# Kernel optimization log

Measured on AMD Instinct MI355X. Metric: run time of the kernel, lower is better.

## Reference

```python
import jax, jax.numpy as jnp
import numpy as np

Q_HEADS, KV_HEADS, DIMS, IN_DIMS = 16, 4, 1024, 1024
HEAD_D = DIMS // Q_HEADS            # 64
GROUPS = Q_HEADS // KV_HEADS        # 4
ROPE_BASE = 10000.0


def nd_rope(x, coords):
    """N-D rotary embedding.
    x: [..., s, d]; coords: broadcastable [..., s, a] (float).
    Head dim d is split into a contiguous chunks of d//a; within each chunk
    consecutive pairs (2i, 2i+1) are rotated by angle coord_axis * base^(-2i/(d//a)).
    """
    a = coords.shape[-1]
    d = x.shape[-1]
    dpa = d // a                                  # dims per coordinate axis (even)
    inv_freq = ROPE_BASE ** (-jnp.arange(dpa // 2, dtype=jnp.float32) * (2.0 / dpa))
    angles = coords[..., :, None] * inv_freq      # [..., s, a, dpa//2]
    angles = angles.reshape(angles.shape[:-2] + (d // 2,))
    cos, sin = jnp.cos(angles), jnp.sin(angles)
    xp = x.reshape(x.shape[:-1] + (d // 2, 2))
    x1, x2 = xp[..., 0], xp[..., 1]
    return jnp.stack([x1 * cos - x2 * sin, x1 * sin + x2 * cos], axis=-1).reshape(x.shape)


def setup_inputs() -> dict:
    key = jax.random.key(0)
    k1, k2, k3, k4, k5, k6, k7, k8 = jax.random.split(key, 8)
    B, SQ, SKV, A = 4, 2048, 2048, 2
    q = jax.random.normal(k1, (B, SQ, IN_DIMS), dtype=jnp.float32)
    kv = jax.random.normal(k2, (B, SKV, IN_DIMS), dtype=jnp.float32)
    q_coords = jax.random.randint(k3, (B, SQ, A), 0, 2048, dtype=jnp.int32)
    kv_coords = jax.random.randint(k4, (B, SKV, A), 0, 2048, dtype=jnp.int32)
    s_in = 1.0 / np.sqrt(IN_DIMS)
    Wq = jax.random.normal(k5, (IN_DIMS, Q_HEADS, HEAD_D), dtype=jnp.float32) * s_in
    Wk = jax.random.normal(k6, (IN_DIMS, KV_HEADS, HEAD_D), dtype=jnp.float32) * s_in
    Wv = jax.random.normal(k7, (IN_DIMS, KV_HEADS, HEAD_D), dtype=jnp.float32) * s_in
    Wo = jax.random.normal(k8, (KV_HEADS * HEAD_D, IN_DIMS), dtype=jnp.float32) * (1.0 / np.sqrt(KV_HEADS * HEAD_D))
    return {"q": q, "q_coords": q_coords, "kv": kv, "kv_coords": kv_coords,
            "Wq": Wq, "Wk": Wk, "Wv": Wv, "Wo": Wo}


def reference(q, q_coords, kv, kv_coords, Wq, Wk, Wv, Wo):
    B, SQ = q.shape[0], q.shape[1]
    qp = jnp.einsum('bsi,ihd->bshd', q, Wq)   # [b, sq, q_heads, hd]
    kp = jnp.einsum('bsi,ihd->bshd', kv, Wk)  # [b, skv, kv_heads, hd]
    vp = jnp.einsum('bsi,ihd->bshd', kv, Wv)
    # '... s (h g) d -> ... g h s d' with h=KV_HEADS outer, g=GROUPS inner
    qp = qp.reshape(B, SQ, KV_HEADS, GROUPS, HEAD_D).transpose(0, 3, 2, 1, 4)  # [b,g,h,sq,hd]
    kp = kp.transpose(0, 2, 1, 3)  # [b,h,skv,hd]
    vp = vp.transpose(0, 2, 1, 3)
    qc = q_coords.astype(jnp.float32)[:, None, None]  # [b,1,1,sq,a] -> broadcast over g,h
    kc = kv_coords.astype(jnp.float32)[:, None]       # [b,1,skv,a] -> broadcast over h
    qr = nd_rope(qp, qc)
    kr = nd_rope(kp, kc)
    # NOTE: einops pattern omits g in output -> group axis is SUMMED (faithful to source)
    scores = jnp.einsum('bghsd,bhad->bhsa', qr, kr) / (HEAD_D ** 0.5)
    attn = jax.nn.softmax(scores, axis=-1)
    out = jnp.einsum('bhsa,bhad->bhsd', attn, vp)
    out = out.transpose(0, 2, 1, 3).reshape(B, SQ, KV_HEADS * HEAD_D)
    return out @ Wo
```

## Files before the change

### kernel.cpp

```cpp
#include <hip/hip_runtime.h>

#define BATCH 4
#define SEQQ  2048
#define SEQKV 2048
#define NH    4
#define HD    64
#define IND   1024
#define QSCL 0.18033688011112042f

typedef __attribute__((ext_vector_type(8))) short short8;
typedef __attribute__((ext_vector_type(4))) short s4v;
typedef __attribute__((ext_vector_type(4))) float floatx4;

#if defined(__HIP_DEVICE_COMPILE__) && __has_builtin(__builtin_amdgcn_exp2f)
  #define EXP2(x) __builtin_amdgcn_exp2f(x)
#else
  #define EXP2(x) exp2f(x)
#endif

#if defined(__HIP_DEVICE_COMPILE__)
  #if __has_builtin(__builtin_amdgcn_mfma_f32_16x16x16bf16_1k)
    #define MFMA16(a, b, c) __builtin_amdgcn_mfma_f32_16x16x16bf16_1k(a, b, c, 0, 0, 0)
  #elif __has_builtin(__builtin_amdgcn_mfma_f32_16x16x16_bf16)
    #define MFMA16(a, b, c) __builtin_amdgcn_mfma_f32_16x16x16_bf16(a, b, c, 0, 0, 0)
  #else
    #error "no 16x16x16 bf16 MFMA builtin on gfx950 device pass"
  #endif
#else
  #define MFMA16(a, b, c) (c)
#endif
#define MFMA32(a, b, c) __builtin_amdgcn_mfma_f32_16x16x32_bf16(a, b, c, 0, 0, 0)

__device__ __forceinline__ short f2b(float f) {
    unsigned u; __builtin_memcpy(&u, &f, 4);
    u = (u + 0x7fffu + ((u >> 16) & 1u)) >> 16;
    return (short)u;
}
__device__ __forceinline__ short8 cvt8(const float* p) {
    float4 a = *(const float4*)p;
    float4 b = *(const float4*)(p + 4);
    short8 r;
    r[0] = f2b(a.x); r[1] = f2b(a.y); r[2] = f2b(a.z); r[3] = f2b(a.w);
    r[4] = f2b(b.x); r[5] = f2b(b.y); r[6] = f2b(b.z); r[7] = f2b(b.w);
    return r;
}

__global__ __launch_bounds__(256) void prep_all(
    const float* __restrict__ Wq, const float* __restrict__ Wk,
    const float* __restrict__ Wv, const float* __restrict__ Wo,
    const float* __restrict__ q, const float* __restrict__ kv,
    short* __restrict__ Wq_t, short* __restrict__ Wkv_t, short* __restrict__ Wo_t,
    short* __restrict__ qb, short* __restrict__ kvb) {
    __shared__ short Ts[64][65];
    int blk = blockIdx.x;
    if (blk < 256) {
        int c4 = threadIdx.x & 63, r4 = threadIdx.x >> 6;
        if (blk < 64) {
            int h = blk & 3, ib = blk >> 2;
#pragma unroll 4
            for (int jj = 0; jj < 16; ++jj) {
                int il = r4 * 16 + jj;
                float s = 0.f;
#pragma unroll
                for (int g = 0; g < 4; ++g)
                    s += Wq[(ib * 64 + il) * 1024 + (h * 4 + g) * 64 + c4];
                Ts[il][c4] = f2b(s);
            }
            __syncthreads();
#pragma unroll 4
            for (int jj = 0; jj < 16; ++jj) {
                int dl = r4 * 16 + jj;
                Wq_t[(h * 64 + dl) * 1024 + ib * 64 + c4] = Ts[c4][dl];
            }
        } else if (blk < 192) {
            int t = blk - 64, ss = t >> 6; t &= 63;
            int ib = t >> 2, nb = t & 3;
            const float* W = ss ? Wv : Wk;
#pragma unroll 4
            for (int jj = 0; jj < 16; ++jj) {
                int il = r4 * 16 + jj;
                Ts[il][c4] = f2b(W[(ib * 64 + il) * 256 + nb * 64 + c4]);
            }
            __syncthreads();
#pragma unroll 4
            for (int jj = 0; jj < 16; ++jj) {
                int dl = r4 * 16 + jj;
                Wkv_t[(ss * 256 + nb * 64 + dl) * 1024 + ib * 64 + c4] = Ts[c4][dl];
            }
        } else {
            int t = blk - 192, kb = t >> 4, nb = t & 15;
#pragma unroll 4
            for (int jj = 0; jj < 16; ++jj) {
                int il = r4 * 16 + jj;
                Ts[il][c4] = f2b(Wo[(kb * 64 + il) * 1024 + nb * 64 + c4]);
            }
            __syncthreads();
#pragma unroll 4
            for (int jj = 0; jj < 16; ++jj) {
                int dl = r4 * 16 + jj;
                Wo_t[(nb * 64 + dl) * 256 + kb * 64 + c4] = Ts[c4][dl];
            }
        }
    } else if (blk < 2304) {
        long e = ((long)(blk - 256) * 256 + threadIdx.x) * 16;
        *(short8*)(qb + e)     = cvt8(q + e);
        *(short8*)(qb + e + 8) = cvt8(q + e + 8);
    } else {
        long e = ((long)(blk - 2304) * 256 + threadIdx.x) * 16;
        *(short8*)(kvb + e)     = cvt8(kv + e);
        *(short8*)(kvb + e + 8) = cvt8(kv + e + 8);
    }
}

template <int MODE>
__device__ __forceinline__ void gemm64(
    const short* __restrict__ A, const short* __restrict__ Wt,
    int m0, int n0, short* As, short* Bs,
    const int* __restrict__ coords, short* __restrict__ ropeDst,
    short* __restrict__ vDst) {
    const int t = threadIdx.x;
    const int w = t >> 6, lane = t & 63, ln = lane & 15, quad = lane >> 4;
    const int srow = lane >> 2, skc = (lane & 3) * 8;
    floatx4 acc[2][4];
#pragma unroll
    for (int mt = 0; mt < 2; ++mt)
#pragma unroll
        for (int nt = 0; nt < 4; ++nt) acc[mt][nt] = floatx4{0.f, 0.f, 0.f, 0.f};

    auto stage = [&](int ks, int sel) {
#pragma unroll
        for (int i = 0; i < 2; ++i)
            __builtin_amdgcn_global_load_lds(
                (const void*)(A + (long)(m0 + w * 32 + i * 16 + srow) * 1024 + ks + skc),
                (void*)(As + sel * 4096 + (w * 2 + i) * 512), 16, 0, 0);
        __builtin_amdgcn_global_load_lds(
            (const void*)(Wt + (long)(n0 + w * 16 + srow) * 1024 + ks + skc),
            (void*)(Bs + sel * 2048 + w * 512), 16, 0, 0);
    };

    stage(0, 0);
    __syncthreads();
    int cur = 0;
    for (int tt = 0; tt < 32; ++tt) {
        if (tt < 31) stage((tt + 1) * 32, cur ^ 1);
        const short* Ac = As + cur * 4096;
        const short* Bc = Bs + cur * 2048;
        short8 af[2], bf[4];
#pragma unroll
        for (int mt = 0; mt < 2; ++mt)
            af[mt] = *(const short8*)(Ac + (w * 32 + mt * 16 + ln) * 32 + quad * 8);
#pragma unroll
        for (int nt = 0; nt < 4; ++nt)
            bf[nt] = *(const short8*)(Bc + (nt * 16 + ln) * 32 + quad * 8);
#pragma unroll
        for (int mt = 0; mt < 2; ++mt)
#pragma unroll
            for (int nt = 0; nt < 4; ++nt)
                acc[mt][nt] = MFMA32(af[mt], bf[nt], acc[mt][nt]);
        __syncthreads();
        cur ^= 1;
    }

    if (MODE == 1 || n0 < 256) {
        const int h = (n0 >> 6) & 3;
        const float scl = (MODE == 1) ? QSCL : 1.0f;
        const float L = -0.5756462732485114f;
        const float fA = __expf((float)(ln >> 1) * L);
        const float fB = __expf((float)(8 + (ln >> 1)) * L);
        const float sgn = (ln & 1) ? 1.0f : -1.0f;
#pragma unroll
        for (int mt = 0; mt < 2; ++mt) {
            int row0 = m0 + w * 32 + mt * 16 + quad * 4;
#pragma unroll
            for (int r = 0; r < 4; ++r) {
                int row = row0 + r;
                float c0 = (float)coords[row * 2];
                float c1 = (float)coords[row * 2 + 1];
                float snv[4], csv[4];
                __sincosf(c0 * fA, &snv[0], &csv[0]);
                __sincosf(c0 * fB, &snv[1], &csv[1]);
                __sincosf(c1 * fA, &snv[2], &csv[2]);
                __sincosf(c1 * fB, &snv[3], &csv[3]);
                long rbase = ((long)((row >> 11) * 4 + h) * 2048 + (row & 2047)) * 64;
#pragma unroll
                for (int nt = 0; nt < 4; ++nt) {
                    float v = acc[mt][nt][r];
                    float p = __shfl_xor(v, 1, 64);
                    float o = v * (csv[nt] * scl) + p * (snv[nt] * (scl * sgn));
                    ropeDst[rbase + nt * 16 + ln] = f2b(o);
                }
            }
        }
    } else {
        const int h = ((n0 - 256) >> 6) & 3;
#pragma unroll
        for (int mt = 0; mt < 2; ++mt) {
            int row0 = m0 + w * 32 + mt * 16 + quad * 4;
            int b = row0 >> 11, s0 = row0 & 2047;
#pragma unroll
            for (int nt = 0; nt < 4; ++nt) {
                s4v ov;
#pragma unroll
                for (int r = 0; r < 4; ++r) ov[r] = f2b(acc[mt][nt][r]);
                *(s4v*)(vDst + (long)((b * 4 + h) * 64 + nt * 16 + ln) * 2048 + s0) = ov;
            }
        }
    }
}

__global__ __launch_bounds__(256) void proj_gemm(
    const short* __restrict__ qb, const short* __restrict__ kvb,
    const short* __restrict__ Wq_t, const short* __restrict__ Wkv_t,
    const int* __restrict__ qc, const int* __restrict__ kvc,
    short* __restrict__ Qr, short* __restrict__ Kr, short* __restrict__ Vt) {
    __shared__ __align__(16) short As[2 * 4096];
    __shared__ __align__(16) short Bs[2 * 2048];
    int id = (blockIdx.x & 7) * 96 + (blockIdx.x >> 3);
    if (id < 256)
        gemm64<1>(qb, Wq_t, (id >> 2) * 128, (id & 3) * 64, As, Bs, qc, Qr, nullptr);
    else {
        int t2 = id - 256;
        gemm64<2>(kvb, Wkv_t, (t2 >> 3) * 128, (t2 & 7) * 64, As, Bs, kvc, Kr, Vt);
    }
}

__global__ __launch_bounds__(256) void final_gemm(
    const short* __restrict__ Ob, const short* __restrict__ Wo_t, float* __restrict__ out) {
    __shared__ __align__(16) short As[2][128 * 32];
    __shared__ __align__(16) short Bs[2][128 * 32];
    const int m0 = blockIdx.x * 128, n0 = blockIdx.y * 128;
    const int tid = threadIdx.x;
    const int w = tid >> 6, lane = tid & 63, ln = lane & 15, quad = lane >> 4;
    const int wm = w >> 1, wn = w & 1;
    const int srow = lane >> 2, skc = (lane & 3) * 8;
    floatx4 acc[4][4];
#pragma unroll
    for (int mt = 0; mt < 4; ++mt)
#pragma unroll
        for (int nt = 0; nt < 4; ++nt) acc[mt][nt] = floatx4{0.f, 0.f, 0.f, 0.f};

    auto stage = [&](int ks, int sel) {
#pragma unroll
        for (int i = 0; i < 2; ++i) {
            __builtin_amdgcn_global_load_lds(
                (const void*)(Ob + (long)(m0 + w * 32 + i * 16 + srow) * 256 + ks + skc),
                (void*)(&As[sel][(w * 2 + i) * 512]), 16, 0, 0);
            __builtin_amdgcn_global_load_lds(
                (const void*)(Wo_t + (long)(n0 + w * 32 + i * 16 + srow) * 256 + ks + skc),
                (void*)(&Bs[sel][(w * 2 + i) * 512]), 16, 0, 0);
        }
    };
    stage(0, 0);
    __syncthreads();
    int cur = 0;
    for (int tt = 0; tt < 8; ++tt) {
        if (tt < 7) stage((tt + 1) * 32, cur ^ 1);
        const short* Ac = &As[cur][0];
        const short* Bc = &Bs[cur][0];
        short8 af[4], bf[4];
#pragma unroll
        for (int mt = 0; mt < 4; ++mt)
            af[mt] = *(const short8*)(Ac + (wm * 64 + mt * 16 + ln) * 32 + quad * 8);
#pragma unroll
        for (int nt = 0; nt < 4; ++nt)
            bf[nt] = *(const short8*)(Bc + (wn * 64 + nt * 16 + ln) * 32 + quad * 8);
#pragma unroll
        for (int mt = 0; mt < 4; ++mt)
#pragma unroll
            for (int nt = 0; nt < 4; ++nt)
                acc[mt][nt] = MFMA32(af[mt], bf[nt], acc[mt][nt]);
        __syncthreads();
        cur ^= 1;
    }
#pragma unroll
    for (int mt = 0; mt < 4; ++mt) {
        int row0 = m0 + wm * 64 + mt * 16 + quad * 4;
#pragma unroll
        for (int nt = 0; nt < 4; ++nt) {
            int col = n0 + wn * 64 + nt * 16 + ln;
#pragma unroll
            for (int r = 0; r < 4; ++r)
                out[(long)(row0 + r) * 1024 + col] = acc[mt][nt][r];
        }
    }
}

__global__ __launch_bounds__(512, 4) void attn_kernel(
    const short* __restrict__ Qr, const short* __restrict__ Kr,
    const short* __restrict__ Vt, short* __restrict__ Ob) {
    __shared__ __align__(16) short Kls[2][2][64 * 64];
    __shared__ __align__(16) short Vls[2][2][64 * 64];
    const int blk = blockIdx.x;
    const int x = blk & 7, y = blk >> 3;
    const int bh = x * 2 + (y >> 5), qg = y & 31;
    const int w = threadIdx.x >> 6, lane = threadIdx.x & 63;
    const int qw = w & 3, half = w >> 2;
    const int ln = lane & 15, quad = lane >> 4;
    const int q0 = qg * 64 + qw * 16;
    const short* Qb = Qr + (long)bh * SEQKV * HD;
    const short* Kb = Kr + (long)bh * SEQKV * HD + (long)half * 1024 * HD;
    const short* Vb = Vt + (long)bh * HD * SEQKV + half * 1024;

    const int srow = lane >> 3;
    const int schk = (lane & 7) ^ (srow & 7);
    const long kstage0 = (long)(qw * 16 + srow) * HD + schk * 8;
    const long vstage0 = (long)(qw * 16 + srow) * SEQKV + schk * 8;

    short8 qf[2];
#pragma unroll
    for (int ck = 0; ck < 2; ++ck)
        qf[ck] = *(const short8*)(Qb + (long)(q0 + ln) * HD + ck * 32 + quad * 8);

    s4v ones;
#pragma unroll
    for (int j = 0; j < 4; ++j) ones[j] = (short)0x3F80;

    floatx4 o[4], ol;
    ol = floatx4{0.f, 0.f, 0.f, 0.f};
#pragma unroll
    for (int nt = 0; nt < 4; ++nt) o[nt] = floatx4{0.f, 0.f, 0.f, 0.f};

    const int ln7 = ln & 7;
    int koff[2];
#pragma unroll
    for (int ck = 0; ck < 2; ++ck) koff[ck] = ln * 64 + ((ck * 4 + quad) ^ ln7) * 8;
    int voff[4];
#pragma unroll
    for (int t = 0; t < 4; ++t) voff[t] = ln * 64 + ((t * 2 + (quad >> 1)) ^ ln7) * 8 + (quad & 1) * 4;

#define STAGE(kt, sel)                                                                \
    do {                                                                              \
        _Pragma("unroll")                                                             \
        for (int i = 0; i < 2; ++i) {                                                 \
            __builtin_amdgcn_global_load_lds(                                         \
                (const void*)(Kb + (long)(kt) * HD + kstage0 + (long)i * 8 * HD),     \
                (void*)(&Kls[half][sel][(qw * 16 + i * 8) * 64]), 16, 0, 0);          \
            __builtin_amdgcn_global_load_lds(                                         \
                (const void*)(Vb + (kt) + vstage0 + (long)i * 8 * SEQKV),             \
                (void*)(&Vls[half][sel][(qw * 16 + i * 8) * 64]), 16, 0, 0);          \
        }                                                                             \
    } while (0)

    STAGE(0, 0);
    __syncthreads();
    int cur = 0;
    for (int tt = 0; tt < 16; ++tt) {
        if (tt < 15) STAGE((tt + 1) * 64, cur ^ 1);
        const short* Kc = &Kls[half][cur][0];
        const short* Vc = &Vls[half][cur][0];
#pragma unroll
        for (int t = 0; t < 4; ++t) {
            short8 a0 = *(const short8*)(Kc + t * 1024 + koff[0]);
            short8 a1 = *(const short8*)(Kc + t * 1024 + koff[1]);
            floatx4 st = {0.f, 0.f, 0.f, 0.f};
            __builtin_amdgcn_s_setprio(1);
            st = MFMA32(a0, qf[0], st);
            st = MFMA32(a1, qf[1], st);
            __builtin_amdgcn_s_setprio(0);
            float e0 = EXP2(st[0]), e1 = EXP2(st[1]), e2 = EXP2(st[2]), e3 = EXP2(st[3]);
            unsigned p0, p1;
            asm("v_cvt_pk_bf16_f32 %0, %1, %2" : "=v"(p0) : "v"(e0), "v"(e1));
            asm("v_cvt_pk_bf16_f32 %0, %1, %2" : "=v"(p1) : "v"(e2), "v"(e3));
            s4v pt;
            { unsigned tmp[2] = {p0, p1}; __builtin_memcpy(&pt, tmp, 8); }
            __builtin_amdgcn_s_setprio(1);
#pragma unroll
            for (int nt = 0; nt < 4; ++nt) {
                s4v vf = *(const s4v*)(Vc + nt * 1024 + voff[t]);
                o[nt] = MFMA16(vf, pt, o[nt]);
            }
            ol = MFMA16(ones, pt, ol);
            __builtin_amdgcn_s_setprio(0);
        }
        __syncthreads();
        cur ^= 1;
    }
#undef STAGE
    float* cb = (float*)&Kls[0][0][0];
    const int slot = (qw * 64 + lane) * 20;
    if (half == 1) {
#pragma unroll
        for (int nt = 0; nt < 4; ++nt)
            *(floatx4*)(cb + slot + nt * 4) = o[nt];
        cb[slot + 16] = ol[0];
    }
    __syncthreads();
    if (half == 0) {
        const int b = bh >> 2, h = bh & 3;
        const float li = 1.0f / (ol[0] + cb[slot + 16]);
        const long base = ((long)(b * 2048 + q0 + ln)) * 256 + h * 64;
#pragma unroll
        for (int nt = 0; nt < 4; ++nt) {
            floatx4 o2 = *(const floatx4*)(cb + slot + nt * 4);
            s4v ov;
#pragma unroll
            for (int r = 0; r < 4; ++r) ov[r] = f2b((o[nt][r] + o2[r]) * li);
            *(s4v*)(Ob + base + nt * 16 + quad * 4) = ov;
        }
    }
}

extern "C" void kernel_launch(void* const* d_in, const int* in_sizes, int n_in,
                              void* d_out, int out_size, void* d_ws, size_t ws_size,
                              hipStream_t stream) {
    const float* q   = (const float*)d_in[0];
    const int*   qc  = (const int*)d_in[1];
    const float* kv  = (const float*)d_in[2];
    const int*   kvc = (const int*)d_in[3];
    const float* Wq  = (const float*)d_in[4];
    const float* Wk  = (const float*)d_in[5];
    const float* Wv  = (const float*)d_in[6];
    const float* Wo  = (const float*)d_in[7];
    float* out = (float*)d_out;

    char* ws = (char*)d_ws;
    const size_t MB = 1024 * 1024;
    short* Wq_t  = (short*)(ws);
    short* Wkv_t = (short*)(ws + MB / 2);
    short* Wo_t  = (short*)(ws + 3 * MB / 2);
    short* qb    = (short*)(ws + 2 * MB);
    short* kvb   = (short*)(ws + 18 * MB);
    short* Qr    = (short*)(ws + 34 * MB);
    short* Kr    = (short*)(ws + 38 * MB);
    short* Vt    = (short*)(ws + 42 * MB);
    short* Ob    = (short*)(ws + 46 * MB);

    hipLaunchKernelGGL(prep_all, dim3(4352), dim3(256), 0, stream,
                       Wq, Wk, Wv, Wo, q, kv, Wq_t, Wkv_t, Wo_t, qb, kvb);
    hipLaunchKernelGGL(proj_gemm, dim3(768), dim3(256), 0, stream,
                       qb, kvb, Wq_t, Wkv_t, qc, kvc, Qr, Kr, Vt);
    hipLaunchKernelGGL(attn_kernel, dim3(512), dim3(512), 0, stream,
                       Qr, Kr, Vt, Ob);
    hipLaunchKernelGGL(final_gemm, dim3(64, 8), dim3(256), 0, stream, Ob, Wo_t, out);
}
```

Baseline: 188.7 us.

## Widen GEMM K-tile to 64 with XOR-swizzled LDS layout in projection and output GEMMs

Both the projection GEMM and the final output GEMM now stage 64-wide K slices instead of 32, which halves the number of main-loop iterations and barriers. The LDS layout gets an XOR swizzle on 16-byte chunks so that the fragment reads avoid bank conflicts. Launch bounds are tightened to fit the doubled shared-memory footprint. The larger LDS use may lower occupancy, and latency hiding now depends on fewer, longer iterations.

Measured after the change: 178.6 us, median of 2. 1.06x faster.

```diff
diff --git a/kernel.cpp b/kernel.cpp
--- a/kernel.cpp
+++ b/kernel.cpp
@@ -120,7 +120,9 @@
     short* __restrict__ vDst) {
     const int t = threadIdx.x;
     const int w = t >> 6, lane = t & 63, ln = lane & 15, quad = lane >> 4;
-    const int srow = lane >> 2, skc = (lane & 3) * 8;
+    const int srow8 = lane >> 3;
+    const int schk = (lane & 7) ^ (srow8 & 7);
+    const int ln7 = ln & 7;
     floatx4 acc[2][4];
 #pragma unroll
     for (int mt = 0; mt < 2; ++mt)
@@ -128,35 +130,45 @@
         for (int nt = 0; nt < 4; ++nt) acc[mt][nt] = floatx4{0.f, 0.f, 0.f, 0.f};
 
     auto stage = [&](int ks, int sel) {
+#pragma unroll
+        for (int i = 0; i < 4; ++i)
+            __builtin_amdgcn_global_load_lds(
+                (const void*)(A + (long)(m0 + w * 32 + i * 8 + srow8) * 1024 + ks + schk * 8),
+                (void*)(As + sel * 8192 + (w * 32 + i * 8) * 64), 16, 0, 0);
 #pragma unroll
         for (int i = 0; i < 2; ++i)
             __builtin_amdgcn_global_load_lds(
-                (const void*)(A + (long)(m0 + w * 32 + i * 16 + srow) * 1024 + ks + skc),
-                (void*)(As + sel * 4096 + (w * 2 + i) * 512), 16, 0, 0);
-        __builtin_amdgcn_global_load_lds(
-            (const void*)(Wt + (long)(n0 + w * 16 + srow) * 1024 + ks + skc),
-            (void*)(Bs + sel * 2048 + w * 512), 16, 0, 0);
+                (const void*)(Wt + (long)(n0 + w * 16 + i * 8 + srow8) * 1024 + ks + schk * 8),
+                (void*)(Bs + sel * 4096 + (w * 16 + i * 8) * 64), 16, 0, 0);
     };
 
     stage(0, 0);
     __syncthreads();
     int cur = 0;
-    for (int tt = 0; tt < 32; ++tt) {
-        if (tt < 31) stage((tt + 1) * 32, cur ^ 1);
-        const short* Ac = As + cur * 4096;
-        const short* Bc = Bs + cur * 2048;
-        short8 af[2], bf[4];
+    for (int tt = 0; tt < 16; ++tt) {
+        if (tt < 15) stage((tt + 1) * 64, cur ^ 1);
+        const short* Ac = As + cur * 8192;
+        const short* Bc = Bs + cur * 4096;
+        short8 af[2][2], bf[4][2];
 #pragma unroll
         for (int mt = 0; mt < 2; ++mt)
-            af[mt] = *(const short8*)(Ac + (w * 32 + mt * 16 + ln) * 32 + quad * 8);
+#pragma unroll
+            for (int kc = 0; kc < 2; ++kc)
+                af[mt][kc] = *(const short8*)(Ac + (w * 32 + mt * 16 + ln) * 64
+                                              + ((kc * 4 + quad) ^ ln7) * 8);
 #pragma unroll
         for (int nt = 0; nt < 4; ++nt)
-            bf[nt] = *(const short8*)(Bc + (nt * 16 + ln) * 32 + quad * 8);
-#pragma unroll
-        for (int mt = 0; mt < 2; ++mt)
-#pragma unroll
-            for (int nt = 0; nt < 4; ++nt)
-                acc[mt][nt] = MFMA32(af[mt], bf[nt], acc[mt][nt]);
+#pragma unroll
+            for (int kc = 0; kc < 2; ++kc)
+                bf[nt][kc] = *(const short8*)(Bc + (nt * 16 + ln) * 64
+                                              + ((kc * 4 + quad) ^ ln7) * 8);
+#pragma unroll
+        for (int kc = 0; kc < 2; ++kc)
+#pragma unroll
+            for (int mt = 0; mt < 2; ++mt)
+#pragma unroll
+                for (int nt = 0; nt < 4; ++nt)
+                    acc[mt][nt] = MFMA32(af[mt][kc], bf[nt][kc], acc[mt][nt]);
         __syncthreads();
         cur ^= 1;
     }
@@ -208,13 +220,13 @@
     }
 }
 
-__global__ __launch_bounds__(256) void proj_gemm(
+__global__ __launch_bounds__(256, 3) void proj_gemm(
     const short* __restrict__ qb, const short* __restrict__ kvb,
     const short* __restrict__ Wq_t, const short* __restrict__ Wkv_t,
     const int* __restrict__ qc, const int* __restrict__ kvc,
     short* __restrict__ Qr, short* __restrict__ Kr, short* __restrict__ Vt) {
-    __shared__ __align__(16) short As[2 * 4096];
-    __shared__ __align__(16) short Bs[2 * 2048];
+    __shared__ __align__(16) short As[2 * 8192];
+    __shared__ __align__(16) short Bs[2 * 4096];
     int id = (blockIdx.x & 7) * 96 + (blockIdx.x >> 3);
     if (id < 256)
         gemm64<1>(qb, Wq_t, (id >> 2) * 128, (id & 3) * 64, As, Bs, qc, Qr, nullptr);
@@ -224,15 +236,17 @@
     }
 }
 
-__global__ __launch_bounds__(256) void final_gemm(
+__global__ __launch_bounds__(256, 2) void final_gemm(
     const short* __restrict__ Ob, const short* __restrict__ Wo_t, float* __restrict__ out) {
-    __shared__ __align__(16) short As[2][128 * 32];
-    __shared__ __align__(16) short Bs[2][128 * 32];
+    __shared__ __align__(16) short As[2 * 8192];
+    __shared__ __align__(16) short Bs[2 * 8192];
     const int m0 = blockIdx.x * 128, n0 = blockIdx.y * 128;
     const int tid = threadIdx.x;
     const int w = tid >> 6, lane = tid & 63, ln = lane & 15, quad = lane >> 4;
     const int wm = w >> 1, wn = w & 1;
-    const int srow = lane >> 2, skc = (lane & 3) * 8;
+    const int srow8 = lane >> 3;
+    const int schk = (lane & 7) ^ (srow8 & 7);
+    const int ln7 = ln & 7;
     floatx4 acc[4][4];
 #pragma unroll
     for (int mt = 0; mt < 4; ++mt)
@@ -241,34 +255,42 @@
 
     auto stage = [&](int ks, int sel) {
 #pragma unroll
-        for (int i = 0; i < 2; ++i) {
+        for (int i = 0; i < 4; ++i) {
             __builtin_amdgcn_global_load_lds(
-                (const void*)(Ob + (long)(m0 + w * 32 + i * 16 + srow) * 256 + ks + skc),
-                (void*)(&As[sel][(w * 2 + i) * 512]), 16, 0, 0);
+                (const void*)(Ob + (long)(m0 + w * 32 + i * 8 + srow8) * 256 + ks + schk * 8),
+                (void*)(As + sel * 8192 + (w * 32 + i * 8) * 64), 16, 0, 0);
             __builtin_amdgcn_global_load_lds(
-                (const void*)(Wo_t + (long)(n0 + w * 32 + i * 16 + srow) * 256 + ks + skc),
-                (void*)(&Bs[sel][(w * 2 + i) * 512]), 16, 0, 0);
+                (const void*)(Wo_t + (long)(n0 + w * 32 + i * 8 + srow8) * 256 + ks + schk * 8),
+                (void*)(Bs + sel * 8192 + (w * 32 + i * 8) * 64), 16, 0, 0);
         }
     };
     stage(0, 0);
     __syncthreads();
     int cur = 0;
-    for (int tt = 0; tt < 8; ++tt) {
-        if (tt < 7) stage((tt + 1) * 32, cur ^ 1);
-        const short* Ac = &As[cur][0];
-        const short* Bc = &Bs[cur][0];
-        short8 af[4], bf[4];
+    for (int tt = 0; tt < 4; ++tt) {
+        if (tt < 3) stage((tt + 1) * 64, cur ^ 1);
+        const short* Ac = As + cur * 8192;
+        const short* Bc = Bs + cur * 8192;
+        short8 af[4][2], bf[4][2];
 #pragma unroll
         for (int mt = 0; mt < 4; ++mt)
-            af[mt] = *(const short8*)(Ac + (wm * 64 + mt * 16 + ln) * 32 + quad * 8);
+#pragma unroll
+            for (int kc = 0; kc < 2; ++kc)
+                af[mt][kc] = *(const short8*)(Ac + (wm * 64 + mt * 16 + ln) * 64
+                                              + ((kc * 4 + quad) ^ ln7) * 8);
 #pragma unroll
         for (int nt = 0; nt < 4; ++nt)
-            bf[nt] = *(const short8*)(Bc + (wn * 64 + nt * 16 + ln) * 32 + quad * 8);
-#pragma unroll
-        for (int mt = 0; mt < 4; ++mt)
-#pragma unroll
-            for (int nt = 0; nt < 4; ++nt)
-                acc[mt][nt] = MFMA32(af[mt], bf[nt], acc[mt][nt]);
+#pragma unroll
+            for (int kc = 0; kc < 2; ++kc)
+                bf[nt][kc] = *(const short8*)(Bc + (wn * 64 + nt * 16 + ln) * 64
+                                              + ((kc * 4 + quad) ^ ln7) * 8);
+#pragma unroll
+        for (int kc = 0; kc < 2; ++kc)
+#pragma unroll
+            for (int mt = 0; mt < 4; ++mt)
+#pragma unroll
+                for (int nt = 0; nt < 4; ++nt)
+                    acc[mt][nt] = MFMA32(af[mt][kc], bf[nt][kc], acc[mt][nt]);
         __syncthreads();
         cur ^= 1;
     }
```
